# Optimization experiments

Hardware: AMD Instinct MI355X
Metric: run time of the kernel (lower is better)

## Reference

```python
import jax, jax.numpy as jnp
import numpy as np

BATCH = 65536
VOCAB = 1048576
EMBED = 128
N_DENSE = 13
N_SPARSE = 26
BOT_DIMS = (512, 256, 128)
TOP_DIMS = (1024, 1024, 512, 256, 1)
TOP_IN = 506  # 128 + 27*28/2


def setup_inputs() -> dict:
    key = jax.random.key(0)
    ks = jax.random.split(key, 32)
    inp = {}
    inp['dense'] = jax.random.normal(ks[0], (BATCH, N_DENSE), dtype=jnp.float32)
    inp['sparse_idx'] = jax.random.randint(ks[1], (BATCH, N_SPARSE), 0, VOCAB, dtype=jnp.int32)
    # embedding table (concatenation of the 4 chunks is mathematically one table)
    scale = 1.0 / np.sqrt(VOCAB)
    inp['emb'] = scale * jax.random.uniform(ks[2], (VOCAB, EMBED), dtype=jnp.float32)
    # bottom MLP params
    fan_in = N_DENSE
    ki = 3
    for i, d in enumerate(BOT_DIMS):
        limit = np.sqrt(6.0 / (fan_in + d))
        inp[f'bw{i}'] = jax.random.uniform(ks[ki], (fan_in, d), jnp.float32, -limit, limit); ki += 1
        inp[f'bb{i}'] = np.sqrt(1.0 / d) * jax.random.normal(ks[ki], (d,), jnp.float32); ki += 1
        fan_in = d
    # top MLP params
    fan_in = TOP_IN
    for i, d in enumerate(TOP_DIMS):
        inp[f'tw{i}'] = np.sqrt(2.0 / (fan_in + d)) * jax.random.normal(ks[ki], (fan_in, d), jnp.float32); ki += 1
        inp[f'tb{i}'] = np.sqrt(1.0 / d) * jax.random.normal(ks[ki], (d,), jnp.float32); ki += 1
        fan_in = d
    return inp


def _triu_idx():
    r, c = np.triu_indices(N_SPARSE + 1)  # includes diagonal, matches torch.triu_indices
    return jnp.asarray(r), jnp.asarray(c)


def reference(dense, sparse_idx, emb,
              bw0, bb0, bw1, bb1, bw2, bb2,
              tw0, tb0, tw1, tb1, tw2, tb2, tw3, tb3, tw4, tb4):
    # bottom MLP
    h = dense
    for w, b in ((bw0, bb0), (bw1, bb1), (bw2, bb2)):
        h = jax.nn.relu(h @ w + b)
    # embedding lookup (modulo as in original)
    idx = jnp.mod(sparse_idx, VOCAB)
    emb_sparse = emb[idx.reshape(-1)].reshape(dense.shape[0], N_SPARSE, EMBED)
    # dot interaction
    combined = jnp.concatenate([h[:, None, :], emb_sparse], axis=1)  # [B, 27, 128]
    inter = jnp.einsum('bnd,bmd->bnm', combined, combined)           # [B, 27, 27]
    r, c = _triu_idx()
    inter_flat = inter[:, r, c]                                      # [B, 378]
    top = jnp.concatenate([h, inter_flat], axis=1)                   # [B, 506]
    # top MLP (ReLU on all but last layer)
    tws = (tw0, tw1, tw2, tw3, tw4)
    tbs = (tb0, tb1, tb2, tb3, tb4)
    for i in range(len(tws)):
        top = top @ tws[i] + tbs[i]
        if i < len(tws) - 1:
            top = jax.nn.relu(top)
    return top  # [B, 1]
```

## Files before the change

### kernel.cpp

```cpp
#include <hip/hip_runtime.h>

#define BATCH 65536
#define NSP 26
#define NROW 27
#define VOCAB_MASK (1048576 - 1)

typedef unsigned short u16;
typedef unsigned int u32;
typedef float f32x4 __attribute__((ext_vector_type(4)));
typedef float f32x16 __attribute__((ext_vector_type(16)));
typedef __bf16 bf16x8 __attribute__((ext_vector_type(8)));

__device__ __forceinline__ u16 f2bf(float f) {
    u32 u = __float_as_uint(f);
    u = (u + 0x7FFFu + ((u >> 16) & 1u)) >> 16;
    return (u16)u;
}
__device__ __forceinline__ float bf2f(u16 h) { return __uint_as_float(((u32)h) << 16); }
__device__ __forceinline__ void fsplit(float x, u16& hi, u16& lo) {
    hi = f2bf(x);
    lo = f2bf(x - bf2f(hi));
}
__device__ __forceinline__ __bf16 u2b(u16 h) { union { u16 u; __bf16 b; } c; c.u = h; return c.b; }

#define GLD16(gp, lp) __builtin_amdgcn_global_load_lds( \
    (const __attribute__((address_space(1))) u32*)(gp), \
    (__attribute__((address_space(3))) u32*)(lp), 16, 0, 0)

__global__ __launch_bounds__(512, 2) void gemm_mfma(
    const u16* __restrict__ Ahi, const u16* __restrict__ Alo,
    const u16* __restrict__ Whi, const u16* __restrict__ Wlo,
    const float* __restrict__ bias,
    u16* __restrict__ Chi, u16* __restrict__ Clo,
    int M, int K, int N, int relu)
{
    __shared__ __align__(16) u16 sbuf[3][24576];

    const int tid = threadIdx.x;
    const int w = tid >> 6, lane = tid & 63;
    const int wr = w >> 1, wc = w & 1;
    const int rl = lane & 31, hl = lane >> 5;

    const int d = blockIdx.y * gridDim.x + blockIdx.x;
    const int nwg = gridDim.x * gridDim.y;
    const int wg = (d & 7) * (nwg >> 3) + (d >> 3);
    const int bx = wg % gridDim.x, by = wg / gridDim.x;
    const int m0 = by * 256, n0 = bx * 128;

    const int nT = K >> 5;

    const u16* gp[6];
    int loff[6], gstr[6];
#pragma unroll
    for (int s = 0; s < 6; ++s) {
        const int u = w * 6 + s;
        if (u < 32) {
            const int uu = u & 15, c = uu >> 2, gq = uu & 3;
            gp[s] = ((u < 16) ? Ahi : Alo) + ((size_t)c * M + m0 + gq * 64 + lane) * 8;
            loff[s] = ((u < 16) ? 0 : 8192) + c * 2048 + gq * 512;
            gstr[s] = M * 32;
        } else {
            const int uu = u & 7, c = uu >> 1, gq = uu & 1;
            gp[s] = ((u < 40) ? Whi : Wlo) + ((size_t)c * N + n0 + gq * 64 + lane) * 8;
            loff[s] = ((u < 40) ? 16384 : 20480) + c * 1024 + gq * 512;
            gstr[s] = N * 32;
        }
    }
    auto stage = [&](int buf) {
        u16* lb = &sbuf[buf][0];
#pragma unroll
        for (int s = 0; s < 6; ++s) {
            GLD16(gp[s], lb + loff[s]);
            gp[s] += gstr[s];
        }
    };

    f32x16 acc[2][2];
#pragma unroll
    for (int i = 0; i < 2; ++i)
#pragma unroll
        for (int j = 0; j < 2; ++j)
#pragma unroll
            for (int r = 0; r < 16; ++r) acc[i][j][r] = 0.f;

    stage(0);
    if (nT > 1) stage(1);

    int bufC = 0;
    for (int t = 0; t < nT; ++t) {
        if (t + 2 < nT) {
            stage((bufC == 0) ? 2 : bufC - 1);
            asm volatile("s_waitcnt vmcnt(12)" ::: "memory");
        } else if (t + 1 < nT) {
            asm volatile("s_waitcnt vmcnt(6)" ::: "memory");
        } else {
            asm volatile("s_waitcnt vmcnt(0)" ::: "memory");
        }
        asm volatile("s_barrier" ::: "memory");

        const u16* sb = sbuf[bufC];
#pragma unroll
        for (int ks = 0; ks < 2; ++ks) {
            const int c = ks * 2 + hl;
            bf16x8 ah[2], al[2], bh[2], blo[2];
#pragma unroll
            for (int i = 0; i < 2; ++i) {
                const int ra = wr * 64 + i * 32 + rl;
                ah[i]  = *(const bf16x8*)&sb[c * 2048 + ra * 8];
                al[i]  = *(const bf16x8*)&sb[8192 + c * 2048 + ra * 8];
                const int rb = wc * 64 + i * 32 + rl;
                bh[i]  = *(const bf16x8*)&sb[16384 + c * 1024 + rb * 8];
                blo[i] = *(const bf16x8*)&sb[20480 + c * 1024 + rb * 8];
            }
#pragma unroll
            for (int i = 0; i < 2; ++i)
#pragma unroll
                for (int j = 0; j < 2; ++j) {
                    f32x16 a = acc[i][j];
                    a = __builtin_amdgcn_mfma_f32_32x32x16_bf16(al[i], bh[j],  a, 0, 0, 0);
                    a = __builtin_amdgcn_mfma_f32_32x32x16_bf16(ah[i], blo[j], a, 0, 0, 0);
                    a = __builtin_amdgcn_mfma_f32_32x32x16_bf16(ah[i], bh[j],  a, 0, 0, 0);
                    acc[i][j] = a;
                }
        }
        asm volatile("s_barrier" ::: "memory");
        bufC = (bufC == 2) ? 0 : bufC + 1;
    }

#pragma unroll
    for (int j = 0; j < 2; ++j) {
        const int n = n0 + wc * 64 + j * 32 + rl;
        const float bs = bias[n];
        const size_t cb = (size_t)(n >> 3) * M * 8 + (n & 7);
#pragma unroll
        for (int i = 0; i < 2; ++i) {
            const int mb = m0 + wr * 64 + i * 32 + 4 * hl;
#pragma unroll
            for (int reg = 0; reg < 16; ++reg) {
                const int row = (reg & 3) + 8 * (reg >> 2);
                float x = acc[i][j][reg] + bs;
                if (relu) x = fmaxf(x, 0.f);
                u16 hi, lo; fsplit(x, hi, lo);
                const size_t off = cb + (size_t)(mb + row) * 8;
                Chi[off] = hi; Clo[off] = lo;
            }
        }
    }
}

__global__ void conv_w(const float* __restrict__ W, u16* __restrict__ Whi,
                       u16* __restrict__ Wlo, int Kreal, int Kpad, int N)
{
    const int idx = blockIdx.x * 256 + threadIdx.x;
    if (idx >= (Kpad >> 3) * N) return;
    const int c = idx / N, n = idx - c * N;
#pragma unroll
    for (int j = 0; j < 8; ++j) {
        const int k = c * 8 + j;
        const float x = (k < Kreal) ? W[(size_t)k * N + n] : 0.f;
        u16 hi, lo; fsplit(x, hi, lo);
        Whi[(size_t)idx * 8 + j] = hi;
        Wlo[(size_t)idx * 8 + j] = lo;
    }
}

__global__ void conv_dense(const float* __restrict__ dense,
                           u16* __restrict__ Dhi, u16* __restrict__ Dlo)
{
    const int m = blockIdx.x * 256 + threadIdx.x;
    float v[13];
#pragma unroll
    for (int j = 0; j < 13; ++j) v[j] = dense[(size_t)m * 13 + j];
#pragma unroll
    for (int cc = 0; cc < 4; ++cc) {
        const size_t base = ((size_t)cc * BATCH + m) * 8;
#pragma unroll
        for (int j = 0; j < 8; ++j) {
            const int k = cc * 8 + j;
            const float x = (k < 13) ? v[k] : 0.f;
            u16 hi, lo; fsplit(x, hi, lo);
            Dhi[base + j] = hi; Dlo[base + j] = lo;
        }
    }
}

__global__ __launch_bounds__(256) void interact_kernel(
    u16* __restrict__ Xhi, u16* __restrict__ Xlo,
    const int* __restrict__ sidx, const float* __restrict__ emb)
{
    const int wave = threadIdx.x >> 6, lane = threadIdx.x & 63;
    const int b = blockIdx.x * 4 + wave;
    const int r = lane & 31, half = lane >> 5;

    bf16x8 fh[8], fl[8];

    if (r == 0) {
#pragma unroll
        for (int s = 0; s < 8; ++s) {
            const size_t base = ((size_t)(2 * s + half) * BATCH + b) * 8;
            fh[s] = *(const bf16x8*)&Xhi[base];
            fl[s] = *(const bf16x8*)&Xlo[base];
        }
    } else if (r <= NSP) {
        const int ix = sidx[(size_t)b * NSP + (r - 1)] & VOCAB_MASK;
        const float* ep = emb + (size_t)ix * 128 + half * 8;
        float4 v[8][2];
#pragma unroll
        for (int s = 0; s < 8; ++s) {
            v[s][0] = *(const float4*)(ep + s * 16);
            v[s][1] = *(const float4*)(ep + s * 16 + 4);
        }
#pragma unroll
        for (int s = 0; s < 8; ++s) {
            const float f[8] = {v[s][0].x, v[s][0].y, v[s][0].z, v[s][0].w,
                                v[s][1].x, v[s][1].y, v[s][1].z, v[s][1].w};
#pragma unroll
            for (int j = 0; j < 8; ++j) {
                u16 hi, lo; fsplit(f[j], hi, lo);
                fh[s][j] = u2b(hi); fl[s][j] = u2b(lo);
            }
        }
    } else {
#pragma unroll
        for (int s = 0; s < 8; ++s) {
#pragma unroll
            for (int j = 0; j < 8; ++j) { fh[s][j] = u2b(0); fl[s][j] = u2b(0); }
        }
    }

    f32x16 acc = {};
#pragma unroll
    for (int s = 0; s < 8; ++s) {
        acc = __builtin_amdgcn_mfma_f32_32x32x16_bf16(fl[s], fh[s], acc, 0, 0, 0);
        acc = __builtin_amdgcn_mfma_f32_32x32x16_bf16(fh[s], fl[s], acc, 0, 0, 0);
        acc = __builtin_amdgcn_mfma_f32_32x32x16_bf16(fh[s], fh[s], acc, 0, 0, 0);
    }

    const int col = lane & 31;
    if (col < NROW) {
#pragma unroll
        for (int reg = 0; reg < 16; ++reg) {
            const int row = (reg & 3) + 8 * (reg >> 2) + 4 * half;
            if (row > col) continue;
            const int k = 128 + row * NROW - (row * (row - 1)) / 2 - row + col;
            u16 hi, lo; fsplit(acc[reg], hi, lo);
            const size_t off = ((size_t)(k >> 3) * BATCH + b) * 8 + (k & 7);
            Xhi[off] = hi; Xlo[off] = lo;
        }
    }
    if (lane < 6) {
        const int k = 506 + lane;
        const size_t off = ((size_t)(k >> 3) * BATCH + b) * 8 + (k & 7);
        Xhi[off] = 0; Xlo[off] = 0;
    }
}

__global__ __launch_bounds__(256) void final_dot(
    const u16* __restrict__ Ahi, const u16* __restrict__ Alo,
    const float* __restrict__ wv, const float* __restrict__ bias,
    float* __restrict__ out)
{
    const int wave = threadIdx.x >> 6, lane = threadIdx.x & 63;
    const int b = blockIdx.x * 4 + wave;
    const int c = lane & 31;
    const u16* src = (lane >= 32) ? Alo : Ahi;
    const size_t base = ((size_t)c * BATCH + b) * 8;
    float s = 0.f;
#pragma unroll
    for (int j = 0; j < 8; ++j) s += bf2f(src[base + j]) * wv[c * 8 + j];
#pragma unroll
    for (int off = 32; off > 0; off >>= 1) s += __shfl_down(s, off);
    if (lane == 0) out[b] = s + bias[0];
}

extern "C" void kernel_launch(void* const* d_in, const int* in_sizes, int n_in,
                              void* d_out, int out_size, void* d_ws, size_t ws_size,
                              hipStream_t stream)
{
    const float* dense = (const float*)d_in[0];
    const int*   sidx  = (const int*)d_in[1];
    const float* emb   = (const float*)d_in[2];
    const float* bw0 = (const float*)d_in[3],  *bb0 = (const float*)d_in[4];
    const float* bw1 = (const float*)d_in[5],  *bb1 = (const float*)d_in[6];
    const float* bw2 = (const float*)d_in[7],  *bb2 = (const float*)d_in[8];
    const float* tw0 = (const float*)d_in[9],  *tb0 = (const float*)d_in[10];
    const float* tw1 = (const float*)d_in[11], *tb1 = (const float*)d_in[12];
    const float* tw2 = (const float*)d_in[13], *tb2 = (const float*)d_in[14];
    const float* tw3 = (const float*)d_in[15], *tb3 = (const float*)d_in[16];
    const float* tw4 = (const float*)d_in[17], *tb4 = (const float*)d_in[18];
    float* out = (float*)d_out;

    char* p = (char*)d_ws;
    const size_t ACT = (size_t)BATCH * 1024 * sizeof(u16);
    u16* Xhi = (u16*)p; p += ACT;
    u16* Xlo = (u16*)p; p += ACT;
    u16* Yhi = (u16*)p; p += ACT;
    u16* Ylo = (u16*)p; p += ACT;
    u16* D0hi = (u16*)p; p += (size_t)BATCH * 32 * sizeof(u16);
    u16* D0lo = (u16*)p; p += (size_t)BATCH * 32 * sizeof(u16);
    auto alloc_w = [&](size_t elems, u16** hi, u16** lo) {
        *hi = (u16*)p; p += elems * sizeof(u16);
        *lo = (u16*)p; p += elems * sizeof(u16);
    };
    u16 *W0h,*W0l,*W1h,*W1l,*W2h,*W2l,*T0h,*T0l,*T1h,*T1l,*T2h,*T2l,*T3h,*T3l;
    alloc_w(32 * 512, &W0h, &W0l);
    alloc_w(512 * 256, &W1h, &W1l);
    alloc_w(256 * 128, &W2h, &W2l);
    alloc_w(512 * 1024, &T0h, &T0l);
    alloc_w(1024 * 1024, &T1h, &T1l);
    alloc_w(1024 * 512, &T2h, &T2l);
    alloc_w(512 * 256, &T3h, &T3l);

    const dim3 blk(256);
    const dim3 gblk(512);
    auto cwg = [](int kpad, int n) { return dim3(((kpad >> 3) * n + 255) / 256); };

    conv_dense<<<BATCH / 256, blk, 0, stream>>>(dense, D0hi, D0lo);
    conv_w<<<cwg(32, 512),    blk, 0, stream>>>(bw0, W0h, W0l, 13,   32,   512);
    conv_w<<<cwg(512, 256),   blk, 0, stream>>>(bw1, W1h, W1l, 512,  512,  256);
    conv_w<<<cwg(256, 128),   blk, 0, stream>>>(bw2, W2h, W2l, 256,  256,  128);
    conv_w<<<cwg(512, 1024),  blk, 0, stream>>>(tw0, T0h, T0l, 506,  512,  1024);
    conv_w<<<cwg(1024, 1024), blk, 0, stream>>>(tw1, T1h, T1l, 1024, 1024, 1024);
    conv_w<<<cwg(1024, 512),  blk, 0, stream>>>(tw2, T2h, T2l, 1024, 1024, 512);
    conv_w<<<cwg(512, 256),   blk, 0, stream>>>(tw3, T3h, T3l, 512,  512,  256);

    gemm_mfma<<<dim3(4, 256), gblk, 0, stream>>>(D0hi, D0lo, W0h, W0l, bb0, Xhi, Xlo, BATCH, 32,  512, 1);
    gemm_mfma<<<dim3(2, 256), gblk, 0, stream>>>(Xhi, Xlo, W1h, W1l, bb1, Yhi, Ylo, BATCH, 512, 256, 1);
    gemm_mfma<<<dim3(1, 256), gblk, 0, stream>>>(Yhi, Ylo, W2h, W2l, bb2, Xhi, Xlo, BATCH, 256, 128, 1);

    interact_kernel<<<dim3(BATCH / 4), blk, 0, stream>>>(Xhi, Xlo, sidx, emb);

    gemm_mfma<<<dim3(8, 256), gblk, 0, stream>>>(Xhi, Xlo, T0h, T0l, tb0, Yhi, Ylo, BATCH, 512,  1024, 1);
    gemm_mfma<<<dim3(8, 256), gblk, 0, stream>>>(Yhi, Ylo, T1h, T1l, tb1, Xhi, Xlo, BATCH, 1024, 1024, 1);
    gemm_mfma<<<dim3(4, 256), gblk, 0, stream>>>(Xhi, Xlo, T2h, T2l, tb2, Yhi, Ylo, BATCH, 1024, 512,  1);
    gemm_mfma<<<dim3(2, 256), gblk, 0, stream>>>(Yhi, Ylo, T3h, T3l, tb3, Xhi, Xlo, BATCH, 512,  256,  1);
    final_dot<<<dim3(BATCH / 4), blk, 0, stream>>>(Xhi, Xlo, tw4, tb4, out);
}
```

Before: 2.097 ms.

## Split GEMM k-loop into two phases interleaving prefetch with MFMA and setprio

Restructures the triple-buffered GEMM main loop into two half-tile phases. Each phase loads its fragments from LDS, then issues half of the next tile's global-to-LDS loads before running the MFMA block. The MFMA block is wrapped in s_setprio(1) and sched barriers, with waitcnt and barriers placed per phase. The aim is to spread memory traffic over the loop and keep the matrix cores busy. The cost is extra barriers per iteration, and the more delicate vmcnt bookkeeping risks correctness or stalls.

```diff
diff --git a/kernel.cpp b/kernel.cpp
--- a/kernel.cpp
+++ b/kernel.cpp
@@ -66,10 +66,10 @@
             gstr[s] = N * 32;
         }
     }
-    auto stage = [&](int buf) {
+    auto stage3 = [&](int buf, int s0) {
         u16* lb = &sbuf[buf][0];
 #pragma unroll
-        for (int s = 0; s < 6; ++s) {
+        for (int s = s0; s < s0 + 3; ++s) {
             GLD16(gp[s], lb + loff[s]);
             gp[s] += gstr[s];
         }
@@ -83,25 +83,23 @@
 #pragma unroll
             for (int r = 0; r < 16; ++r) acc[i][j][r] = 0.f;
 
-    stage(0);
-    if (nT > 1) stage(1);
+    stage3(0, 0); stage3(0, 3);
+    if (nT > 1) {
+        stage3(1, 0); stage3(1, 3);
+        asm volatile("s_waitcnt vmcnt(6)" ::: "memory");
+    } else {
+        asm volatile("s_waitcnt vmcnt(0)" ::: "memory");
+    }
+    asm volatile("s_barrier" ::: "memory");
 
     int bufC = 0;
     for (int t = 0; t < nT; ++t) {
-        if (t + 2 < nT) {
-            stage((bufC == 0) ? 2 : bufC - 1);
-            asm volatile("s_waitcnt vmcnt(12)" ::: "memory");
-        } else if (t + 1 < nT) {
-            asm volatile("s_waitcnt vmcnt(6)" ::: "memory");
-        } else {
-            asm volatile("s_waitcnt vmcnt(0)" ::: "memory");
-        }
-        asm volatile("s_barrier" ::: "memory");
-
         const u16* sb = sbuf[bufC];
-#pragma unroll
-        for (int ks = 0; ks < 2; ++ks) {
-            const int c = ks * 2 + hl;
+        const int bufN2 = (bufC == 0) ? 2 : bufC - 1;
+        const bool pf = (t + 2 < nT);
+
+        {
+            const int c = hl;
             bf16x8 ah[2], al[2], bh[2], blo[2];
 #pragma unroll
             for (int i = 0; i < 2; ++i) {
@@ -112,6 +110,11 @@
                 bh[i]  = *(const bf16x8*)&sb[16384 + c * 1024 + rb * 8];
                 blo[i] = *(const bf16x8*)&sb[20480 + c * 1024 + rb * 8];
             }
+            if (pf) stage3(bufN2, 0);
+            asm volatile("s_barrier" ::: "memory");
+            asm volatile("s_waitcnt lgkmcnt(0)" ::: "memory");
+            __builtin_amdgcn_sched_barrier(0);
+            __builtin_amdgcn_s_setprio(1);
 #pragma unroll
             for (int i = 0; i < 2; ++i)
 #pragma unroll
@@ -122,8 +125,43 @@
                     a = __builtin_amdgcn_mfma_f32_32x32x16_bf16(ah[i], bh[j],  a, 0, 0, 0);
                     acc[i][j] = a;
                 }
-        }
-        asm volatile("s_barrier" ::: "memory");
+            __builtin_amdgcn_s_setprio(0);
+            asm volatile("s_barrier" ::: "memory");
+        }
+
+        {
+            const int c = 2 + hl;
+            bf16x8 ah[2], al[2], bh[2], blo[2];
+#pragma unroll
+            for (int i = 0; i < 2; ++i) {
+                const int ra = wr * 64 + i * 32 + rl;
+                ah[i]  = *(const bf16x8*)&sb[c * 2048 + ra * 8];
+                al[i]  = *(const bf16x8*)&sb[8192 + c * 2048 + ra * 8];
+                const int rb = wc * 64 + i * 32 + rl;
+                bh[i]  = *(const bf16x8*)&sb[16384 + c * 1024 + rb * 8];
+                blo[i] = *(const bf16x8*)&sb[20480 + c * 1024 + rb * 8];
+            }
+            if (pf) stage3(bufN2, 3);
+            if (pf)                 asm volatile("s_waitcnt vmcnt(6)" ::: "memory");
+            else if (t + 1 < nT)    asm volatile("s_waitcnt vmcnt(0)" ::: "memory");
+            asm volatile("s_barrier" ::: "memory");
+            asm volatile("s_waitcnt lgkmcnt(0)" ::: "memory");
+            __builtin_amdgcn_sched_barrier(0);
+            __builtin_amdgcn_s_setprio(1);
+#pragma unroll
+            for (int i = 0; i < 2; ++i)
+#pragma unroll
+                for (int j = 0; j < 2; ++j) {
+                    f32x16 a = acc[i][j];
+                    a = __builtin_amdgcn_mfma_f32_32x32x16_bf16(al[i], bh[j],  a, 0, 0, 0);
+                    a = __builtin_amdgcn_mfma_f32_32x32x16_bf16(ah[i], blo[j], a, 0, 0, 0);
+                    a = __builtin_amdgcn_mfma_f32_32x32x16_bf16(ah[i], bh[j],  a, 0, 0, 0);
+                    acc[i][j] = a;
+                }
+            __builtin_amdgcn_s_setprio(0);
+            asm volatile("s_barrier" ::: "memory");
+        }
+
         bufC = (bufC == 2) ? 0 : bufC + 1;
     }
 
```

Result: no change. 2.110 ms (+0.6%).
